# Kernel tuning notes

Measured on AMD Instinct MI355X. Metric: run time of the kernel, lower is better.

The kernel has to match this reference:

```python
import jax, jax.numpy as jnp
import numpy as np

EPS_GEN = 1e-7   # GENConv message epsilon
LN_EPS = 1e-5    # torch LayerNorm default eps


def _ln(x, g, b):
    mu = x.mean(-1, keepdims=True)
    v = ((x - mu) ** 2).mean(-1, keepdims=True)
    return (x - mu) / jnp.sqrt(v + LN_EPS) * g + b


def _genconv(x, src, dst, N, t, W1, b1, g1, be1, W2, b2):
    # GENConv(aggr='softmax', learn_t, num_layers=2, norm='layer'), no edge_attr
    msg = jax.nn.relu(x[src]) + EPS_GEN                 # [E,H] gather + eps
    z = msg * t
    m = jax.ops.segment_max(z, dst, num_segments=N)      # scatter-max [N,H]
    e = jnp.exp(z - m[dst])
    denom = jax.ops.segment_sum(e, dst, num_segments=N) + 1e-16
    alpha = e / denom[dst]                               # per-neighborhood softmax
    out = jax.ops.segment_sum(msg * alpha, dst, num_segments=N) + x  # aggregate + root
    h = jax.nn.relu(_ln(out @ W1 + b1, g1, be1))         # MLP [H,2H] + LN + ReLU
    return h @ W2 + b2                                   # [2H,H] plain last layer


def setup_inputs():
    key = jax.random.key(0)
    ks = jax.random.split(key, 24)
    N, E, Fin, H = 100000, 1600000, 16, 64
    s = 0.02
    d = {
        'x': jax.random.normal(ks[0], (N, Fin), jnp.float32),
        'edge_index': jax.random.randint(ks[1], (2, E), 0, N, dtype=jnp.int32),
        'W_enc': jax.random.normal(ks[2], (Fin, H), jnp.float32) * s,
        'b_enc': jnp.zeros((H,), jnp.float32),
        't1': jnp.float32(1.0),
        'W1a': jax.random.normal(ks[3], (H, 2 * H), jnp.float32) * s,
        'b1a': jnp.zeros((2 * H,), jnp.float32),
        'g1a': jnp.ones((2 * H,), jnp.float32),
        'be1a': jnp.zeros((2 * H,), jnp.float32),
        'W1b': jax.random.normal(ks[4], (2 * H, H), jnp.float32) * s,
        'b1b': jnp.zeros((H,), jnp.float32),
        'g_n1': jnp.ones((H,), jnp.float32),
        'b_n1': jnp.zeros((H,), jnp.float32),
        't2': jnp.float32(1.0),
        'W2a': jax.random.normal(ks[5], (H, 2 * H), jnp.float32) * s,
        'b2a': jnp.zeros((2 * H,), jnp.float32),
        'g2a': jnp.ones((2 * H,), jnp.float32),
        'be2a': jnp.zeros((2 * H,), jnp.float32),
        'W2b': jax.random.normal(ks[6], (2 * H, H), jnp.float32) * s,
        'b2b': jnp.zeros((H,), jnp.float32),
        'g_n0': jnp.ones((H,), jnp.float32),
        'b_n0': jnp.zeros((H,), jnp.float32),
        'W_lin': jax.random.normal(ks[7], (H, 1), jnp.float32) * s,
        'b_lin': jnp.zeros((1,), jnp.float32),
    }
    return d


def reference(x, edge_index, W_enc, b_enc, t1, W1a, b1a, g1a, be1a, W1b, b1b,
              g_n1, b_n1, t2, W2a, b2a, g2a, be2a, W2b, b2b, g_n0, b_n0,
              W_lin, b_lin):
    N = x.shape[0]
    src, dst = edge_index[0], edge_index[1]
    h = x @ W_enc + b_enc                                   # node encoder
    h = _genconv(h, src, dst, N, t1, W1a, b1a, g1a, be1a, W1b, b1b)  # layers[0].conv (bare)
    # layers[1]: DeepGCNLayer res+ -> x + conv(act(norm(x)))  (dropout = identity, deterministic ref)
    r = _genconv(jax.nn.relu(_ln(h, g_n1, b_n1)), src, dst, N, t2,
                 W2a, b2a, g2a, be2a, W2b, b2b)
    h = h + r
    h = jax.nn.relu(_ln(h, g_n0, b_n0))                     # layers[0].norm / act at the end
    logits = h @ W_lin + b_lin                              # [N,1]
    return jax.nn.sigmoid(logits), logits
```

## Files before the change

### kernel.cpp

```cpp
#include <hip/hip_runtime.h>
#include <hip/hip_fp16.h>
#include <math.h>

constexpr int HD   = 64;
constexpr int HD2  = 128;
constexpr int SCAP = 48;
constexpr int NPW  = 4;
constexpr int NPB  = 16;
constexpr int PSH  = 14;
constexpr int EPB  = 2048;

constexpr int SO = 68;
constexpr int SU = 132;
constexpr int SY = 68;

constexpr float FXS  = 8192.f;
constexpr float FXSI = 1.f / 8192.f;
constexpr float RXS  = 16384.f;
constexpr float RXSI = 1.f / 16384.f;
constexpr float HXS  = 4096.f;
constexpr float HXSI = 1.f / 4096.f;

#if __has_builtin(__builtin_amdgcn_exp2f)
#define FEXP2(x) __builtin_amdgcn_exp2f(x)
#define EXP_SCALE 1.4426950408889634f
#else
#define FEXP2(x) __expf(x)
#define EXP_SCALE 1.0f
#endif

typedef short  bf16x8 __attribute__((ext_vector_type(8)));
typedef float  f32x4  __attribute__((ext_vector_type(4)));

__device__ __forceinline__ float wave_sum(float v) {
#pragma unroll
    for (int off = 32; off > 0; off >>= 1) v += __shfl_xor(v, off, 64);
    return v;
}

__device__ __forceinline__ unsigned short packm(float v) {
    int q = (int)(fmaxf(v, 0.f) * FXS + 0.5f);
    return (unsigned short)min(q, 65535);
}

__device__ __forceinline__ short f2s16(float v, float s) {
    int q = (int)rintf(v * s);
    return (short)max(-32768, min(32767, q));
}

__device__ __forceinline__ void splitf(float f, short& hi, short& lo) {
    unsigned u = __float_as_uint(f);
    hi = (short)(u >> 16);
    float lf = f - __uint_as_float(u & 0xffff0000u);
    lo = (short)(__float_as_uint(lf) >> 16);
}

__device__ __forceinline__ void split8(const float* p, bf16x8& hi, bf16x8& lo) {
    float v[8];
    *(float4*)&v[0] = *(const float4*)p;
    *(float4*)&v[4] = *(const float4*)(p + 4);
#pragma unroll
    for (int j = 0; j < 8; j++) { short h, l; splitf(v[j], h, l); hi[j] = h; lo[j] = l; }
}

__global__ void prep_kernel(const int* __restrict__ ei,
                            int* __restrict__ cursor, int* __restrict__ slots,
                            const float* __restrict__ x,
                            const float* __restrict__ W,
                            const float* __restrict__ b,
                            short* __restrict__ h0s,
                            unsigned short* __restrict__ g,
                            const float* __restrict__ L1W1, const float* __restrict__ L1W2,
                            const float* __restrict__ L2W1, const float* __restrict__ L2W2,
                            short* __restrict__ swz,
                            int E, int N, int SB, int encB) {
    if (blockIdx.x < (unsigned)SB) {
        int chunks = SB >> 3;
        int p  = blockIdx.x / chunks;
        int ck = blockIdx.x - p * chunks;
        int e0 = ck * EPB + threadIdx.x;
        int d8[8], s8[8];
#pragma unroll
        for (int it = 0; it < 8; it++) {
            int e = e0 + it * 256;
            bool v = (e < E);
            d8[it] = v ? ei[E + e] : -1;
            s8[it] = v ? ei[e] : 0;
        }
#pragma unroll
        for (int it = 0; it < 8; it++) {
            int dst = d8[it];
            if (dst >= 0 && (dst >> PSH) == p) {
                int pos = atomicAdd(&cursor[dst], 1);
                if (pos < SCAP) slots[(unsigned)(dst * SCAP + pos)] = s8[it];
            }
        }
    } else if (blockIdx.x < (unsigned)(SB + encB)) {
        int i = (blockIdx.x - SB) * 256 + threadIdx.x;
        if (i >= N * HD) return;
        int n = i >> 6, j = i & 63;
        const float* xr = x + (unsigned)(n * 16);
        float acc = b[j];
#pragma unroll
        for (int k = 0; k < 16; k++) acc += xr[k] * W[k * HD + j];
        h0s[i] = f2s16(acc, RXS);
        g[i] = packm(acc);
    } else {
        int sb = blockIdx.x - SB - encB;
        int layer = sb >> 3;
        int idx = (sb & 7) * 256 + threadIdx.x;
        const float* Wa = layer ? L2W1 : L1W1;
        const float* Wb = layer ? L2W2 : L1W2;
        short* base = swz + layer * 32768;
        if (idx < 1024) {
            int ks = idx >> 9, rem = idx & 511;
            int nt = rem >> 6, lane = rem & 63;
#pragma unroll
            for (int j = 0; j < 8; j++) {
                int k = ks * 32 + (lane >> 4) * 8 + j;
                int n = nt * 16 + (lane & 15);
                short hh, ll; splitf(Wa[k * HD2 + n], hh, ll);
                base[idx * 8 + j] = hh; base[8192 + idx * 8 + j] = ll;
            }
        } else {
            int jdx = idx - 1024;
            int ks = jdx >> 8, rem = jdx & 255;
            int nt = rem >> 6, lane = rem & 63;
#pragma unroll
            for (int j = 0; j < 8; j++) {
                int k = ks * 32 + (lane >> 4) * 8 + j;
                int n = nt * 16 + (lane & 15);
                short hh, ll; splitf(Wb[k * HD + n], hh, ll);
                base[16384 + jdx * 8 + j] = hh; base[24576 + jdx * 8 + j] = ll;
            }
        }
    }
}

template <int MODE>
__global__ void __launch_bounds__(256) conv_kernel(
    const unsigned short* __restrict__ gin,
    const short* __restrict__ hroot,
    const int* __restrict__ deg_arr, const int* __restrict__ slots,
    const float* __restrict__ tcur,
    const short* __restrict__ W1hi, const short* __restrict__ W1lo,
    const float* __restrict__ b1,
    const float* __restrict__ g1, const float* __restrict__ be1,
    const short* __restrict__ W2hi, const short* __restrict__ W2lo,
    const float* __restrict__ b2,
    const float* __restrict__ gn, const float* __restrict__ bn,
    const short* __restrict__ resid,
    const float* __restrict__ wlin, const float* __restrict__ blin,
    float* __restrict__ outA, short* __restrict__ outH,
    unsigned short* __restrict__ outG, int N) {
    __shared__ float s_out[NPB][SO];
    __shared__ float s_u[NPB][SU];
    __shared__ float s_y[NPB][SY];
    int wv = threadIdx.x >> 6, j = threadIdx.x & 63;
    int q = j >> 4;
    int c = (j & 15) << 2;
    int nb = blockIdx.x * NPB + wv * NPW;
    float cexp = tcur[0] * (FXSI * EXP_SCALE);

    int deg[NPW], sid[NPW];
#pragma unroll
    for (int u = 0; u < NPW; u++) {
        int n = nb + u;
        int d = (n < N) ? min(deg_arr[n], SCAP) : 0;
        deg[u] = d;
        sid[u] = (j < d) ? slots[(unsigned)(n * SCAP + j)] : 0;
    }
#pragma unroll
    for (int u = 0; u < NPW; u++) {
        int n = nb + u;
        int bl = wv * NPW + u;
        if (n < N) {
            int d = deg[u];
            float4 ae = {0.f, 0.f, 0.f, 0.f}, aw = {0.f, 0.f, 0.f, 0.f};
            for (int base = 0; base < d; base += 16) {
                uint2 uv[4];
#pragma unroll
                for (int bb = 0; bb < 4; bb++) {
                    int i = base + bb * 4 + q;
                    int s = __shfl(sid[u], i, 64);
                    uv[bb] = *(const uint2*)(gin + (unsigned)((s << 6) | c));
                }
#pragma unroll
                for (int bb = 0; bb < 4; bb++) {
                    int i = base + bb * 4 + q;
                    if (i < d) {
                        uint2 w = uv[bb];
                        float m0 = (float)(w.x & 0xffffu), m1 = (float)(w.x >> 16);
                        float m2 = (float)(w.y & 0xffffu), m3 = (float)(w.y >> 16);
                        float e0 = FEXP2(m0 * cexp);
                        float e1 = FEXP2(m1 * cexp);
                        float e2 = FEXP2(m2 * cexp);
                        float e3 = FEXP2(m3 * cexp);
                        ae.x += e0; ae.y += e1; ae.z += e2; ae.w += e3;
                        aw.x = fmaf(m0, e0, aw.x); aw.y = fmaf(m1, e1, aw.y);
                        aw.z = fmaf(m2, e2, aw.z); aw.w = fmaf(m3, e3, aw.w);
                    }
                }
            }
#pragma unroll
            for (int off = 16; off <= 32; off <<= 1) {
                ae.x += __shfl_xor(ae.x, off, 64); ae.y += __shfl_xor(ae.y, off, 64);
                ae.z += __shfl_xor(ae.z, off, 64); ae.w += __shfl_xor(ae.w, off, 64);
                aw.x += __shfl_xor(aw.x, off, 64); aw.y += __shfl_xor(aw.y, off, 64);
                aw.z += __shfl_xor(aw.z, off, 64); aw.w += __shfl_xor(aw.w, off, 64);
            }
            if (q == 0) {
                float4 o;
                float n0 = fmaf(ae.x, 1e-7f, aw.x * FXSI);
                float n1 = fmaf(ae.y, 1e-7f, aw.y * FXSI);
                float n2 = fmaf(ae.z, 1e-7f, aw.z * FXSI);
                float n3 = fmaf(ae.w, 1e-7f, aw.w * FXSI);
                if (MODE == 0) {
                    short4 hv = *(const short4*)(hroot + (unsigned)((n << 6) | c));
                    o.x = n0 / (ae.x + 1e-16f) + (float)hv.x * RXSI;
                    o.y = n1 / (ae.y + 1e-16f) + (float)hv.y * RXSI;
                    o.z = n2 / (ae.z + 1e-16f) + (float)hv.z * RXSI;
                    o.w = n3 / (ae.w + 1e-16f) + (float)hv.w * RXSI;
                } else {
                    ushort4 rv = *(const ushort4*)(gin + (unsigned)((n << 6) | c));
                    o.x = n0 / (ae.x + 1e-16f) + (float)rv.x * FXSI;
                    o.y = n1 / (ae.y + 1e-16f) + (float)rv.y * FXSI;
                    o.z = n2 / (ae.z + 1e-16f) + (float)rv.z * FXSI;
                    o.w = n3 / (ae.w + 1e-16f) + (float)rv.w * FXSI;
                }
                *(float4*)&s_out[bl][c] = o;
            }
        } else if (q == 0) {
            float4 z = {0.f, 0.f, 0.f, 0.f};
            *(float4*)&s_out[bl][c] = z;
        }
    }
    __syncthreads();

    int mrow = j & 15, kq = j >> 4, ncol = j & 15;
    {
        f32x4 acc[2];
#pragma unroll
        for (int i = 0; i < 2; i++) {
            float bb = b1[(wv * 2 + i) * 16 + ncol];
            acc[i] = (f32x4){bb, bb, bb, bb};
        }
#pragma unroll
        for (int ks = 0; ks < 2; ks++) {
            bf16x8 ah, al;
            split8(&s_out[mrow][ks * 32 + kq * 8], ah, al);
#pragma unroll
            for (int i = 0; i < 2; i++) {
                int nt = wv * 2 + i;
                int fo = (((ks * 8 + nt) * 64 + j) << 3);
                bf16x8 bh = *(const bf16x8*)(W1hi + fo);
                bf16x8 bl = *(const bf16x8*)(W1lo + fo);
                acc[i] = __builtin_amdgcn_mfma_f32_16x16x32_bf16(al, bh, acc[i], 0, 0, 0);
                acc[i] = __builtin_amdgcn_mfma_f32_16x16x32_bf16(ah, bl, acc[i], 0, 0, 0);
                acc[i] = __builtin_amdgcn_mfma_f32_16x16x32_bf16(ah, bh, acc[i], 0, 0, 0);
            }
        }
#pragma unroll
        for (int i = 0; i < 2; i++)
#pragma unroll
            for (int r = 0; r < 4; r++)
                s_u[kq * 4 + r][(wv * 2 + i) * 16 + ncol] = acc[i][r];
    }
    __syncthreads();

    {
        float g1a_ = g1[j], g1b_ = g1[HD + j];
        float be1a_ = be1[j], be1b_ = be1[HD + j];
#pragma unroll
        for (int u = 0; u < NPW; u++) {
            int bl = wv * NPW + u;
            float u0 = s_u[bl][j], u1 = s_u[bl][HD + j];
            float mu = wave_sum(u0 + u1) * (1.f / HD2);
            float d0 = u0 - mu, d1 = u1 - mu;
            float var = wave_sum(d0 * d0 + d1 * d1) * (1.f / HD2);
            float rstd = rsqrtf(var + 1e-5f);
            s_u[bl][j]      = fmaxf(d0 * rstd * g1a_ + be1a_, 0.f);
            s_u[bl][HD + j] = fmaxf(d1 * rstd * g1b_ + be1b_, 0.f);
        }
    }
    __syncthreads();

    {
        float bb = b2[wv * 16 + ncol];
        f32x4 acc = (f32x4){bb, bb, bb, bb};
#pragma unroll
        for (int ks = 0; ks < 4; ks++) {
            bf16x8 ah, al;
            split8(&s_u[mrow][ks * 32 + kq * 8], ah, al);
            int fo = (((ks * 4 + wv) * 64 + j) << 3);
            bf16x8 bh = *(const bf16x8*)(W2hi + fo);
            bf16x8 bl = *(const bf16x8*)(W2lo + fo);
            acc = __builtin_amdgcn_mfma_f32_16x16x32_bf16(al, bh, acc, 0, 0, 0);
            acc = __builtin_amdgcn_mfma_f32_16x16x32_bf16(ah, bl, acc, 0, 0, 0);
            acc = __builtin_amdgcn_mfma_f32_16x16x32_bf16(ah, bh, acc, 0, 0, 0);
        }
#pragma unroll
        for (int r = 0; r < 4; r++)
            s_y[kq * 4 + r][wv * 16 + ncol] = acc[r];
    }
    __syncthreads();

    float gn_ = gn[j], bn_ = bn[j];
    float wl = (MODE == 1) ? wlin[j] : 0.f;
#pragma unroll
    for (int u = 0; u < NPW; u++) {
        int n = nb + u;
        if (n >= N) continue;
        float yv = s_y[wv * NPW + u][j];
        unsigned oidx = (unsigned)((n << 6) | j);
        if (MODE == 0) {
            outH[oidx] = f2s16(yv, HXS);
            float mu = wave_sum(yv) * (1.f / HD);
            float d = yv - mu;
            float var = wave_sum(d * d) * (1.f / HD);
            float rstd = rsqrtf(var + 1e-5f);
            outG[oidx] = packm(d * rstd * gn_ + bn_);
        } else {
            float hf = yv + (float)resid[oidx] * HXSI;
            float mu = wave_sum(hf) * (1.f / HD);
            float d = hf - mu;
            float var = wave_sum(d * d) * (1.f / HD);
            float rstd = rsqrtf(var + 1e-5f);
            float h2 = fmaxf(d * rstd * gn_ + bn_, 0.f);
            float dot = wave_sum(h2 * wl);
            if (j == 0) {
                float logit = dot + blin[0];
                outA[n] = 1.f / (1.f + __expf(-logit));
                outA[N + n] = logit;
            }
        }
    }
}

extern "C" void kernel_launch(void* const* d_in, const int* in_sizes, int n_in,
                              void* d_out, int out_size, void* d_ws, size_t ws_size,
                              hipStream_t stream) {
    const float* x     = (const float*)d_in[0];
    const int*   ei    = (const int*)  d_in[1];
    const float* W_enc = (const float*)d_in[2];
    const float* b_enc = (const float*)d_in[3];
    const float* t1    = (const float*)d_in[4];
    const float* W1a   = (const float*)d_in[5];
    const float* b1a   = (const float*)d_in[6];
    const float* g1a   = (const float*)d_in[7];
    const float* be1a  = (const float*)d_in[8];
    const float* W1b   = (const float*)d_in[9];
    const float* b1b   = (const float*)d_in[10];
    const float* g_n1  = (const float*)d_in[11];
    const float* b_n1  = (const float*)d_in[12];
    const float* t2    = (const float*)d_in[13];
    const float* W2a   = (const float*)d_in[14];
    const float* b2a   = (const float*)d_in[15];
    const float* g2a   = (const float*)d_in[16];
    const float* be2a  = (const float*)d_in[17];
    const float* W2b   = (const float*)d_in[18];
    const float* b2b   = (const float*)d_in[19];
    const float* g_n0  = (const float*)d_in[20];
    const float* b_n0  = (const float*)d_in[21];
    const float* W_lin = (const float*)d_in[22];
    const float* b_lin = (const float*)d_in[23];

    int N = in_sizes[0] / 16;
    int E = in_sizes[1] / 2;
    size_t NH = (size_t)N * HD;

    short* h0s          = (short*)d_ws;
    short* h1s          = h0s + NH;
    unsigned short* g0  = (unsigned short*)(h1s + NH);
    unsigned short* g1f = g0 + NH;
    int*   cursor       = (int*)(g1f + NH);
    int*   slots        = cursor + N;
    short* swz          = (short*)(slots + (size_t)N * SCAP);

    int nodeBlocks = (N + NPB - 1) / NPB;
    int chunks     = (E + EPB - 1) / EPB;
    int SB         = chunks * 8;
    int encBlocks  = (int)((NH + 255) / 256);

    hipMemsetAsync(cursor, 0, (size_t)N * sizeof(int), stream);

    prep_kernel<<<SB + encBlocks + 16, 256, 0, stream>>>(
        ei, cursor, slots, x, W_enc, b_enc, h0s, g0,
        W1a, W1b, W2a, W2b, swz, E, N, SB, encBlocks);

    short* W1hi_1 = swz,          *W1lo_1 = swz + 8192;
    short* W2hi_1 = swz + 16384,  *W2lo_1 = swz + 24576;
    short* W1hi_2 = swz + 32768,  *W1lo_2 = swz + 40960;
    short* W2hi_2 = swz + 49152,  *W2lo_2 = swz + 57344;

    conv_kernel<0><<<nodeBlocks, 256, 0, stream>>>(
        g0, h0s, cursor, slots, t1,
        W1hi_1, W1lo_1, b1a, g1a, be1a, W2hi_1, W2lo_1, b1b,
        g_n1, b_n1, nullptr, nullptr, nullptr,
        nullptr, h1s, g1f, N);

    conv_kernel<1><<<nodeBlocks, 256, 0, stream>>>(
        g1f, nullptr, cursor, slots, t2,
        W1hi_2, W1lo_2, b2a, g2a, be2a, W2hi_2, W2lo_2, b2b,
        g_n0, b_n0, h1s, W_lin, b_lin,
        (float*)d_out, nullptr, nullptr, N);
}
```

Before: 396.9 us.

## Drop destination-partitioned edge scatter; use flat atomic insert and coarser encoder blocks

The edge-bucketing phase no longer has each chunk of edges read 8 times by 8 blocks that each handle one destination partition. Each edge is now read once and inserted with a single atomic on its destination cursor, and each thread handles 4 edges. The encoder blocks also process 8 elements per thread, which cuts the block count. The change removes 8x redundant edge-index reads at the cost of losing the destination locality of the atomics and slot writes, which the old partitioning was meant to keep within an L2-friendly range.

```diff
diff --git a/kernel.cpp b/kernel.cpp
--- a/kernel.cpp
+++ b/kernel.cpp
@@ -7,8 +7,8 @@
 constexpr int SCAP = 48;
 constexpr int NPW  = 4;
 constexpr int NPB  = 16;
-constexpr int PSH  = 14;
-constexpr int EPB  = 2048;
+constexpr int EPT  = 4;
+constexpr int ENCF = 8;
 
 constexpr int SO = 68;
 constexpr int SU = 132;
@@ -75,36 +75,38 @@
                             short* __restrict__ swz,
                             int E, int N, int SB, int encB) {
     if (blockIdx.x < (unsigned)SB) {
-        int chunks = SB >> 3;
-        int p  = blockIdx.x / chunks;
-        int ck = blockIdx.x - p * chunks;
-        int e0 = ck * EPB + threadIdx.x;
-        int d8[8], s8[8];
-#pragma unroll
-        for (int it = 0; it < 8; it++) {
+        int e0 = blockIdx.x * (256 * EPT) + threadIdx.x;
+        int d4[EPT], s4[EPT];
+#pragma unroll
+        for (int it = 0; it < EPT; it++) {
             int e = e0 + it * 256;
             bool v = (e < E);
-            d8[it] = v ? ei[E + e] : -1;
-            s8[it] = v ? ei[e] : 0;
-        }
-#pragma unroll
-        for (int it = 0; it < 8; it++) {
-            int dst = d8[it];
-            if (dst >= 0 && (dst >> PSH) == p) {
+            d4[it] = v ? ei[E + e] : -1;
+            s4[it] = v ? ei[e] : 0;
+        }
+#pragma unroll
+        for (int it = 0; it < EPT; it++) {
+            int dst = d4[it];
+            if (dst >= 0) {
                 int pos = atomicAdd(&cursor[dst], 1);
-                if (pos < SCAP) slots[(unsigned)(dst * SCAP + pos)] = s8[it];
+                if (pos < SCAP) slots[(unsigned)dst * SCAP + pos] = s4[it];
             }
         }
     } else if (blockIdx.x < (unsigned)(SB + encB)) {
-        int i = (blockIdx.x - SB) * 256 + threadIdx.x;
-        if (i >= N * HD) return;
-        int n = i >> 6, j = i & 63;
-        const float* xr = x + (unsigned)(n * 16);
-        float acc = b[j];
-#pragma unroll
-        for (int k = 0; k < 16; k++) acc += xr[k] * W[k * HD + j];
-        h0s[i] = f2s16(acc, RXS);
-        g[i] = packm(acc);
+        int ibase = (blockIdx.x - SB) * (256 * ENCF) + threadIdx.x;
+#pragma unroll
+        for (int it = 0; it < ENCF; it++) {
+            int i = ibase + it * 256;
+            if (i < N * HD) {
+                int n = i >> 6, j = i & 63;
+                const float* xr = x + (unsigned)(n * 16);
+                float acc = b[j];
+#pragma unroll
+                for (int k = 0; k < 16; k++) acc += xr[k] * W[k * HD + j];
+                h0s[i] = f2s16(acc, RXS);
+                g[i] = packm(acc);
+            }
+        }
     } else {
         int sb = blockIdx.x - SB - encB;
         int layer = sb >> 3;
@@ -378,9 +380,8 @@
     short* swz          = (short*)(slots + (size_t)N * SCAP);
 
     int nodeBlocks = (N + NPB - 1) / NPB;
-    int chunks     = (E + EPB - 1) / EPB;
-    int SB         = chunks * 8;
-    int encBlocks  = (int)((NH + 255) / 256);
+    int SB         = (E + 256 * EPT - 1) / (256 * EPT);
+    int encBlocks  = (int)((NH + 256 * ENCF - 1) / (256 * ENCF));
 
     hipMemsetAsync(cursor, 0, (size_t)N * sizeof(int), stream);
 
```

Result: slower. 451.1 us (+13.6%).
